# Performance work log

Hardware: AMD Instinct MI355X
Metric: run time of the kernel (lower is better)

## Reference

```python
import jax, jax.numpy as jnp
import numpy as np

LN_EPS = 1e-5

def _layernorm(x, g, b):
    m = jnp.mean(x, axis=-1, keepdims=True)
    v = jnp.var(x, axis=-1, keepdims=True)
    return (x - m) * jax.lax.rsqrt(v + LN_EPS) * g + b

def setup_inputs() -> dict:
    key = jax.random.key(0)
    ks = jax.random.split(key, 12)
    BT, D, OH, OW = 32, 768, 28, 43
    N, NFB, NFC = 12, 1024, 256
    s = 0.02
    return {
        "roi_feature": jax.random.normal(ks[0], (BT * N, NFB), jnp.float32),
        "image_feature": jax.random.normal(ks[1], (BT, D, OH, OW), jnp.float32),
        "conv_w": jax.random.normal(ks[2], (NFC, D), jnp.float32) * s,
        "conv_b": jnp.zeros((NFC,), jnp.float32),
        "emb_w": jax.random.normal(ks[3], (NFC, NFB), jnp.float32) * s,
        "emb_b": jnp.zeros((NFC,), jnp.float32),
        "ln1_g": jnp.ones((NFC,), jnp.float32),
        "ln1_b": jnp.zeros((NFC,), jnp.float32),
        "ffn_w1": jax.random.normal(ks[4], (NFC, NFC), jnp.float32) * s,
        "ffn_b1": jnp.zeros((NFC,), jnp.float32),
        "ffn_w2": jax.random.normal(ks[5], (NFC, NFC), jnp.float32) * s,
        "ffn_b2": jnp.zeros((NFC,), jnp.float32),
        "ln2_g": jnp.ones((NFC,), jnp.float32),
        "ln2_b": jnp.zeros((NFC,), jnp.float32),
        "N": 12,
        "layer_id": 1,
    }

def reference(roi_feature, image_feature, conv_w, conv_b, emb_w, emb_b,
              ln1_g, ln1_b, ffn_w1, ffn_b1, ffn_w2, ffn_b2, ln2_g, ln2_b,
              N, layer_id):
    BT, D, OH, OW = image_feature.shape
    NFC = conv_w.shape[0]
    # 1x1 conv == channel GEMM: [BT, D, OH, OW] -> [BT, NFC, OH*OW]
    img = jnp.einsum('bchw,oc->bohw', image_feature, conv_w) + conv_b[None, :, None, None]
    img = img.reshape(BT, NFC, OH * OW)                       # [BT, NFC, P]
    # roi embedding: [BT*N, NFB] -> [BT, N, NFC]
    emb = (roi_feature @ emb_w.T + emb_b).reshape(BT, N, NFC)
    # cross-attention: logits [BT, N, P], softmax over spatial positions
    logits = jnp.einsum('bnc,bcp->bnp', emb, img)
    A = jax.nn.softmax(logits, axis=2)
    ctx = jnp.einsum('bnp,bcp->bnc', A, img).reshape(BT * N, NFC)
    # residual + LN1 (dropout is identity at inference)
    x = _layernorm(ctx + emb.reshape(BT * N, NFC), ln1_g, ln1_b)
    # FFN residual + LN2
    h = jax.nn.relu(x @ ffn_w1.T + ffn_b1) @ ffn_w2.T + ffn_b2
    return _layernorm(x + h, ln2_g, ln2_b)
```

## Files before the change

### kernel.cpp

```cpp
#include <hip/hip_runtime.h>
#include <hip/hip_bf16.h>
#include <stdint.h>

typedef __hip_bfloat16 bf16;
typedef __attribute__((ext_vector_type(8))) __bf16 frag8;
typedef __attribute__((ext_vector_type(4))) float f32x4;

__device__ inline float wred_sum(float v) {
#pragma unroll
  for (int o = 32; o; o >>= 1) v += __shfl_down(v, o);
  return v;
}
__device__ inline float wred_max(float v) {
#pragma unroll
  for (int o = 32; o; o >>= 1) v = fmaxf(v, __shfl_down(v, o));
  return v;
}
__device__ inline unsigned short bits_of(bf16 h) { return *(unsigned short*)&h; }
__device__ inline frag8 cvt8(float4 lo, float4 hi) {
  union { frag8 f; unsigned short u[8]; } r;
  r.u[0] = bits_of(__float2bfloat16(lo.x));
  r.u[1] = bits_of(__float2bfloat16(lo.y));
  r.u[2] = bits_of(__float2bfloat16(lo.z));
  r.u[3] = bits_of(__float2bfloat16(lo.w));
  r.u[4] = bits_of(__float2bfloat16(hi.x));
  r.u[5] = bits_of(__float2bfloat16(hi.y));
  r.u[6] = bits_of(__float2bfloat16(hi.z));
  r.u[7] = bits_of(__float2bfloat16(hi.w));
  return r.f;
}

__global__ __launch_bounds__(256) void wt_k(const float* __restrict__ W,
                                            bf16* __restrict__ Wt) {
  __shared__ float t[32][33];
  int c0 = blockIdx.x * 32, o0 = blockIdx.y * 32;
  int tx = threadIdx.x & 31, ty = threadIdx.x >> 5;
#pragma unroll
  for (int i = 0; i < 4; ++i)
    t[ty + i * 8][tx] = W[(long)(o0 + ty + i * 8) * 768 + c0 + tx];
  __syncthreads();
#pragma unroll
  for (int i = 0; i < 4; ++i)
    Wt[(long)(c0 + ty + i * 8) * 256 + o0 + tx] = __float2bfloat16(t[tx][ty + i * 8]);
}

template <int NT, bool AF32, bool BF32, bool RELU, bool OUT_BF16, bool BIAS>
__global__ __launch_bounds__(64) void gemm_sm2(const void* __restrict__ Av,
                                               const void* __restrict__ Bv,
                                               void* __restrict__ C, int K, int ldc,
                                               const float* __restrict__ bias) {
  int n0 = blockIdx.x * (16 * NT), m0 = blockIdx.y * 64;
  int lr = threadIdx.x & 15, kg = threadIdx.x >> 4;
  f32x4 acc[4][NT] = {};
#pragma unroll 2
  for (int k0 = 0; k0 < K; k0 += 32) {
    frag8 af[4], bv[NT];
#pragma unroll
    for (int mi = 0; mi < 4; ++mi) {
      long row = m0 + mi * 16 + lr;
      if constexpr (AF32) {
        const float* ap = (const float*)Av + row * K + k0 + kg * 8;
        af[mi] = cvt8(*(const float4*)ap, *(const float4*)(ap + 4));
      } else {
        af[mi] = *(const frag8*)((const bf16*)Av + row * K + k0 + kg * 8);
      }
    }
#pragma unroll
    for (int ni = 0; ni < NT; ++ni) {
      long row = n0 + ni * 16 + lr;
      if constexpr (BF32) {
        const float* bp = (const float*)Bv + row * K + k0 + kg * 8;
        bv[ni] = cvt8(*(const float4*)bp, *(const float4*)(bp + 4));
      } else {
        bv[ni] = *(const frag8*)((const bf16*)Bv + row * K + k0 + kg * 8);
      }
    }
#pragma unroll
    for (int mi = 0; mi < 4; ++mi)
#pragma unroll
      for (int ni = 0; ni < NT; ++ni)
        acc[mi][ni] = __builtin_amdgcn_mfma_f32_16x16x32_bf16(af[mi], bv[ni],
                                                              acc[mi][ni], 0, 0, 0);
  }
#pragma unroll
  for (int mi = 0; mi < 4; ++mi)
#pragma unroll
    for (int ni = 0; ni < NT; ++ni)
#pragma unroll
      for (int j = 0; j < 4; ++j) {
        int row = m0 + mi * 16 + kg * 4 + j;
        int col = n0 + ni * 16 + lr;
        float v = acc[mi][ni][j];
        if (BIAS) v += bias[col];
        if (RELU) v = fmaxf(v, 0.f);
        long idx = (long)row * ldc + col;
        if constexpr (OUT_BF16) ((bf16*)C)[idx] = __float2bfloat16(v);
        else ((float*)C)[idx] = v;
      }
}

__global__ __launch_bounds__(256) void logits2(const float* __restrict__ X,
                                               const float* __restrict__ embW,
                                               float* __restrict__ lgt) {
  int px = blockIdx.x, cs = blockIdx.y, b = blockIdx.z;
  __shared__ float e[12 * 96];
  for (int i = threadIdx.x; i < 12 * 96; i += 256)
    e[i] = embW[((long)b * 12 + i / 96) * 768 + cs * 96 + (i % 96)];
  __syncthreads();
  int slot = px * 256 + threadIdx.x;
  if (slot >= 301) return;
  int p = slot * 4;
  const float* xb = X + ((long)b * 768 + cs * 96) * 1204 + p;
  float a0[12], a1[12], a2[12], a3[12];
#pragma unroll
  for (int n = 0; n < 12; ++n) { a0[n] = a1[n] = a2[n] = a3[n] = 0.f; }
#pragma unroll 4
  for (int c = 0; c < 96; ++c) {
    float4 xq = *(const float4*)(xb + (long)c * 1204);
#pragma unroll
    for (int n = 0; n < 12; ++n) {
      float en = e[n * 96 + c];
      a0[n] += en * xq.x; a1[n] += en * xq.y;
      a2[n] += en * xq.z; a3[n] += en * xq.w;
    }
  }
#pragma unroll
  for (int n = 0; n < 12; ++n)
    *(float4*)&lgt[((long)cs * 384 + b * 12 + n) * 1204 + p] =
        make_float4(a0[n], a1[n], a2[n], a3[n]);
}

__global__ __launch_bounds__(256) void softmax2(const float* __restrict__ lgt,
                                                bf16* __restrict__ am) {
  const long PS = (long)384 * 1204;
  int b = blockIdx.x, n = blockIdx.y, tid = threadIdx.x;
  bf16* row = am + ((long)b * 16 + n) * 1280;
  if (n >= 12) {
    for (int i = tid; i < 1280; i += 256) row[i] = __float2bfloat16(0.f);
    return;
  }
  const float* l0 = lgt + ((long)b * 12 + n) * 1204;
  float vals[5];
  float m = -3.0e38f;
#pragma unroll
  for (int i = 0; i < 5; ++i) {
    int pp = tid + i * 256;
    if (pp < 1204) {
      float v = 0.f;
#pragma unroll
      for (int q = 0; q < 8; ++q) v += l0[q * PS + pp];
      vals[i] = v;
    } else {
      vals[i] = -3.0e38f;
    }
    m = fmaxf(m, vals[i]);
  }
  m = wred_max(m);
  __shared__ float rd[4];
  int w = tid >> 6, lane = tid & 63;
  if (lane == 0) rd[w] = m;
  __syncthreads();
  m = fmaxf(fmaxf(rd[0], rd[1]), fmaxf(rd[2], rd[3]));
  float s = 0.f;
#pragma unroll
  for (int i = 0; i < 5; ++i) {
    int pp = tid + i * 256;
    vals[i] = (pp < 1204) ? __expf(vals[i] - m) : 0.f;
    s += vals[i];
  }
  s = wred_sum(s);
  __syncthreads();
  if (lane == 0) rd[w] = s;
  __syncthreads();
  s = rd[0] + rd[1] + rd[2] + rd[3];
  float inv = 1.f / s;
#pragma unroll
  for (int i = 0; i < 5; ++i) {
    int pp = tid + i * 256;
    row[pp] = __float2bfloat16((pp < 1204) ? vals[i] * inv : 0.f);
  }
}

__global__ __launch_bounds__(64) void ctx_a(const float* __restrict__ X,
                                            const bf16* __restrict__ am,
                                            float* __restrict__ Yp) {
  int ct = blockIdx.x, kc = blockIdx.y, b = blockIdx.z;
  int c0 = ct * 64;
  int kst = kc * 256, kend = min(kst + 256, 1204);
  int lr = threadIdx.x & 15, kg = threadIdx.x >> 4;
  f32x4 acc[4] = {};
  for (int k0 = kst; k0 < kend; k0 += 32) {
    frag8 bv = *(const frag8*)(am + ((long)b * 16 + lr) * 1280 + k0 + kg * 8);
    bool full = (k0 + 32 <= 1204);
#pragma unroll
    for (int mi = 0; mi < 4; ++mi) {
      const float* ap = X + ((long)b * 768 + c0 + mi * 16 + lr) * 1204 + k0 + kg * 8;
      frag8 av;
      if (full) {
        av = cvt8(*(const float4*)ap, *(const float4*)(ap + 4));
      } else {
        float t[8];
#pragma unroll
        for (int j = 0; j < 8; ++j)
          t[j] = (k0 + kg * 8 + j < 1204) ? ap[j] : 0.f;
        av = cvt8(make_float4(t[0], t[1], t[2], t[3]),
                  make_float4(t[4], t[5], t[6], t[7]));
      }
      acc[mi] = __builtin_amdgcn_mfma_f32_16x16x32_bf16(av, bv, acc[mi], 0, 0, 0);
    }
  }
  if (lr < 12) {
#pragma unroll
    for (int mi = 0; mi < 4; ++mi) {
      long base = (((long)kc * 32 + b) * 12 + lr) * 768 + c0 + mi * 16 + kg * 4;
      *(float4*)&Yp[base] = make_float4(acc[mi][0], acc[mi][1], acc[mi][2], acc[mi][3]);
    }
  }
}

__global__ __launch_bounds__(256) void red_y(const float* __restrict__ Yp,
                                             bf16* __restrict__ Ysum) {
  const long QS = (long)32 * 12 * 768;
  long i = ((long)blockIdx.x * 256 + threadIdx.x) * 4;
  if (i >= QS) return;
  float4 v = *(const float4*)(Yp + i);
#pragma unroll
  for (int q = 1; q < 5; ++q) {
    float4 u = *(const float4*)(Yp + q * QS + i);
    v.x += u.x; v.y += u.y; v.z += u.z; v.w += u.w;
  }
  union { ushort4 s; bf16 h[4]; } o;
  o.h[0] = __float2bfloat16(v.x);
  o.h[1] = __float2bfloat16(v.y);
  o.h[2] = __float2bfloat16(v.z);
  o.h[3] = __float2bfloat16(v.w);
  *(ushort4*)(Ysum + i) = o.s;
}

__global__ __launch_bounds__(256) void ln_k(const float* __restrict__ a,
                                            const float* __restrict__ bb,
                                            const float* __restrict__ g,
                                            const float* __restrict__ be,
                                            float* __restrict__ of) {
  int r = blockIdx.x, c = threadIdx.x;
  long idx = (long)r * 256 + c;
  float v = a[idx] + bb[idx];
  float s = wred_sum(v);
  float s2 = wred_sum(v * v);
  __shared__ float r1[4], r2[4];
  int w = c >> 6, lane = c & 63;
  if (lane == 0) { r1[w] = s; r2[w] = s2; }
  __syncthreads();
  float st = r1[0] + r1[1] + r1[2] + r1[3];
  float s2t = r2[0] + r2[1] + r2[2] + r2[3];
  float mean = st * (1.f / 256.f);
  float var = s2t * (1.f / 256.f) - mean * mean;
  float rs = rsqrtf(var + 1e-5f);
  of[idx] = (v - mean) * rs * g[c] + be[c];
}

extern "C" void kernel_launch(void* const* d_in, const int* in_sizes, int n_in,
                              void* d_out, int out_size, void* d_ws, size_t ws_size,
                              hipStream_t stream) {
  const float* roi   = (const float*)d_in[0];
  const float* imgf  = (const float*)d_in[1];
  const float* convw = (const float*)d_in[2];
  const float* convb = (const float*)d_in[3];
  const float* embw  = (const float*)d_in[4];
  const float* embb  = (const float*)d_in[5];
  const float* ln1g  = (const float*)d_in[6];
  const float* ln1b  = (const float*)d_in[7];
  const float* w1    = (const float*)d_in[8];
  const float* b1    = (const float*)d_in[9];
  const float* w2    = (const float*)d_in[10];
  const float* b2    = (const float*)d_in[11];
  const float* ln2g  = (const float*)d_in[12];
  const float* ln2b  = (const float*)d_in[13];
  float* out = (float*)d_out;

  char* p = (char*)d_ws;
  size_t off = 0;
  auto take = [&](size_t sz) -> char* {
    char* r = p + off;
    off += (sz + 255) & ~(size_t)255;
    return r;
  };
  float* emb  = (float*)take((size_t)384 * 256 * 4);
  bf16*  Wt   = (bf16*)take((size_t)768 * 256 * 2);
  float* embW = (float*)take((size_t)384 * 768 * 4);
  float* lgt  = (float*)take((size_t)8 * 384 * 1204 * 4);
  bf16*  am   = (bf16*)take((size_t)32 * 16 * 1280 * 2);
  float* Yp   = (float*)take((size_t)5 * 32 * 12 * 768 * 4);
  bf16*  Ysum = (bf16*)take((size_t)384 * 768 * 2);
  float* ctxf = (float*)take((size_t)384 * 256 * 4);
  float* x    = (float*)take((size_t)384 * 256 * 4);
  bf16*  h1   = (bf16*)take((size_t)384 * 256 * 2);
  float* h    = (float*)take((size_t)384 * 256 * 4);

  gemm_sm2<1, true, true, false, false, true><<<dim3(16, 6), 64, 0, stream>>>(
      roi, embw, emb, 1024, 256, embb);
  wt_k<<<dim3(24, 8), 256, 0, stream>>>(convw, Wt);
  gemm_sm2<1, true, false, false, false, false><<<dim3(48, 6), 64, 0, stream>>>(
      emb, Wt, embW, 256, 768, nullptr);
  logits2<<<dim3(2, 8, 32), 256, 0, stream>>>(imgf, embW, lgt);
  softmax2<<<dim3(32, 16), 256, 0, stream>>>(lgt, am);
  ctx_a<<<dim3(12, 5, 32), 64, 0, stream>>>(imgf, am, Yp);
  red_y<<<288, 256, 0, stream>>>(Yp, Ysum);
  gemm_sm2<1, false, true, false, false, true><<<dim3(16, 6), 64, 0, stream>>>(
      Ysum, convw, ctxf, 768, 256, convb);
  ln_k<<<384, 256, 0, stream>>>(ctxf, emb, ln1g, ln1b, x);
  gemm_sm2<1, true, true, true, true, true><<<dim3(16, 6), 64, 0, stream>>>(
      x, w1, h1, 256, 256, b1);
  gemm_sm2<1, false, true, false, false, true><<<dim3(16, 6), 64, 0, stream>>>(
      h1, w2, h, 256, 256, b2);
  ln_k<<<384, 256, 0, stream>>>(h, x, ln2g, ln2b, out);
}
```

Measured before the change: 137.8 us.

## Fuse tail GEMMs and layernorms into one kernel; split logits channels finer

Replaces the five tail launches (conv GEMM, LN1, two FFN GEMMs, LN2) with one tail_k kernel. Each block handles 16 rows, keeps intermediates in LDS and converts the fp32 weights to bf16 on the fly. The logits kernel now splits channels into 16 chunks of 48 with 320-thread blocks (one block per batch and chunk instead of two), so softmax sums 16 partials. This removes launch overhead and global round-trips for the tail, but tail_k runs only 24 blocks, which may underuse the GPU, and the logits change doubles the partial-sum traffic.

```diff
diff --git a/kernel.cpp b/kernel.cpp
--- a/kernel.cpp
+++ b/kernel.cpp
@@ -44,17 +44,17 @@
     Wt[(long)(c0 + ty + i * 8) * 256 + o0 + tx] = __float2bfloat16(t[tx][ty + i * 8]);
 }
 
-template <int NT, bool AF32, bool BF32, bool RELU, bool OUT_BF16, bool BIAS>
+template <bool AF32, bool BF32, bool BIAS>
 __global__ __launch_bounds__(64) void gemm_sm2(const void* __restrict__ Av,
                                                const void* __restrict__ Bv,
-                                               void* __restrict__ C, int K, int ldc,
+                                               float* __restrict__ C, int K, int ldc,
                                                const float* __restrict__ bias) {
-  int n0 = blockIdx.x * (16 * NT), m0 = blockIdx.y * 64;
+  int n0 = blockIdx.x * 16, m0 = blockIdx.y * 64;
   int lr = threadIdx.x & 15, kg = threadIdx.x >> 4;
-  f32x4 acc[4][NT] = {};
+  f32x4 acc[4] = {};
 #pragma unroll 2
   for (int k0 = 0; k0 < K; k0 += 32) {
-    frag8 af[4], bv[NT];
+    frag8 af[4], bv;
 #pragma unroll
     for (int mi = 0; mi < 4; ++mi) {
       long row = m0 + mi * 16 + lr;
@@ -65,61 +65,52 @@
         af[mi] = *(const frag8*)((const bf16*)Av + row * K + k0 + kg * 8);
       }
     }
-#pragma unroll
-    for (int ni = 0; ni < NT; ++ni) {
-      long row = n0 + ni * 16 + lr;
+    {
+      long row = n0 + lr;
       if constexpr (BF32) {
         const float* bp = (const float*)Bv + row * K + k0 + kg * 8;
-        bv[ni] = cvt8(*(const float4*)bp, *(const float4*)(bp + 4));
+        bv = cvt8(*(const float4*)bp, *(const float4*)(bp + 4));
       } else {
-        bv[ni] = *(const frag8*)((const bf16*)Bv + row * K + k0 + kg * 8);
+        bv = *(const frag8*)((const bf16*)Bv + row * K + k0 + kg * 8);
       }
     }
 #pragma unroll
     for (int mi = 0; mi < 4; ++mi)
-#pragma unroll
-      for (int ni = 0; ni < NT; ++ni)
-        acc[mi][ni] = __builtin_amdgcn_mfma_f32_16x16x32_bf16(af[mi], bv[ni],
-                                                              acc[mi][ni], 0, 0, 0);
+      acc[mi] = __builtin_amdgcn_mfma_f32_16x16x32_bf16(af[mi], bv, acc[mi], 0, 0, 0);
   }
 #pragma unroll
   for (int mi = 0; mi < 4; ++mi)
 #pragma unroll
-    for (int ni = 0; ni < NT; ++ni)
-#pragma unroll
-      for (int j = 0; j < 4; ++j) {
-        int row = m0 + mi * 16 + kg * 4 + j;
-        int col = n0 + ni * 16 + lr;
-        float v = acc[mi][ni][j];
-        if (BIAS) v += bias[col];
-        if (RELU) v = fmaxf(v, 0.f);
-        long idx = (long)row * ldc + col;
-        if constexpr (OUT_BF16) ((bf16*)C)[idx] = __float2bfloat16(v);
-        else ((float*)C)[idx] = v;
-      }
-}
-
-__global__ __launch_bounds__(256) void logits2(const float* __restrict__ X,
+    for (int j = 0; j < 4; ++j) {
+      int row = m0 + mi * 16 + kg * 4 + j;
+      int col = n0 + lr;
+      float v = acc[mi][j];
+      if (BIAS) v += bias[col];
+      C[(long)row * ldc + col] = v;
+    }
+}
+
+__global__ __launch_bounds__(320) void logits2(const float* __restrict__ X,
                                                const float* __restrict__ embW,
                                                float* __restrict__ lgt) {
-  int px = blockIdx.x, cs = blockIdx.y, b = blockIdx.z;
-  __shared__ float e[12 * 96];
-  for (int i = threadIdx.x; i < 12 * 96; i += 256)
-    e[i] = embW[((long)b * 12 + i / 96) * 768 + cs * 96 + (i % 96)];
-  __syncthreads();
-  int slot = px * 256 + threadIdx.x;
+  int cs = blockIdx.x, b = blockIdx.y;
+  __shared__ float e[12 * 48];
+  for (int i = threadIdx.x; i < 12 * 48; i += 320)
+    e[i] = embW[((long)b * 12 + i / 48) * 768 + cs * 48 + (i % 48)];
+  __syncthreads();
+  int slot = threadIdx.x;
   if (slot >= 301) return;
   int p = slot * 4;
-  const float* xb = X + ((long)b * 768 + cs * 96) * 1204 + p;
+  const float* xb = X + ((long)b * 768 + cs * 48) * 1204 + p;
   float a0[12], a1[12], a2[12], a3[12];
 #pragma unroll
   for (int n = 0; n < 12; ++n) { a0[n] = a1[n] = a2[n] = a3[n] = 0.f; }
 #pragma unroll 4
-  for (int c = 0; c < 96; ++c) {
+  for (int c = 0; c < 48; ++c) {
     float4 xq = *(const float4*)(xb + (long)c * 1204);
 #pragma unroll
     for (int n = 0; n < 12; ++n) {
-      float en = e[n * 96 + c];
+      float en = e[n * 48 + c];
       a0[n] += en * xq.x; a1[n] += en * xq.y;
       a2[n] += en * xq.z; a3[n] += en * xq.w;
     }
@@ -148,7 +139,7 @@
     if (pp < 1204) {
       float v = 0.f;
 #pragma unroll
-      for (int q = 0; q < 8; ++q) v += l0[q * PS + pp];
+      for (int q = 0; q < 16; ++q) v += l0[q * PS + pp];
       vals[i] = v;
     } else {
       vals[i] = -3.0e38f;
@@ -237,26 +228,135 @@
   *(ushort4*)(Ysum + i) = o.s;
 }
 
-__global__ __launch_bounds__(256) void ln_k(const float* __restrict__ a,
-                                            const float* __restrict__ bb,
-                                            const float* __restrict__ g,
-                                            const float* __restrict__ be,
-                                            float* __restrict__ of) {
-  int r = blockIdx.x, c = threadIdx.x;
-  long idx = (long)r * 256 + c;
-  float v = a[idx] + bb[idx];
-  float s = wred_sum(v);
-  float s2 = wred_sum(v * v);
-  __shared__ float r1[4], r2[4];
-  int w = c >> 6, lane = c & 63;
-  if (lane == 0) { r1[w] = s; r2[w] = s2; }
-  __syncthreads();
-  float st = r1[0] + r1[1] + r1[2] + r1[3];
-  float s2t = r2[0] + r2[1] + r2[2] + r2[3];
-  float mean = st * (1.f / 256.f);
-  float var = s2t * (1.f / 256.f) - mean * mean;
-  float rs = rsqrtf(var + 1e-5f);
-  of[idx] = (v - mean) * rs * g[c] + be[c];
+__global__ __launch_bounds__(256) void tail_k(
+    const bf16* __restrict__ Ysum, const float* __restrict__ convw,
+    const float* __restrict__ convb, const float* __restrict__ emb,
+    const float* __restrict__ ln1g, const float* __restrict__ ln1b,
+    const float* __restrict__ w1, const float* __restrict__ b1,
+    const float* __restrict__ w2, const float* __restrict__ b2,
+    const float* __restrict__ ln2g, const float* __restrict__ ln2b,
+    float* __restrict__ out) {
+  int r0 = blockIdx.x * 16;
+  __shared__ __align__(16) bf16 A_l[16][776];
+  __shared__ float x_l[16][260];
+  __shared__ __align__(16) bf16 xb_l[16][264];
+  __shared__ __align__(16) bf16 h1_l[16][264];
+  int tid = threadIdx.x;
+  int lane = tid & 63, w = tid >> 6;
+  int lr = lane & 15, kg = lane >> 4;
+  int n0 = w * 64;
+  for (int i = tid; i < 1536; i += 256) {
+    int r = i / 96, c8 = (i % 96) * 8;
+    *(uint4*)&A_l[r][c8] = *(const uint4*)(Ysum + (long)(r0 + r) * 768 + c8);
+  }
+  __syncthreads();
+  {
+    f32x4 acc[4] = {};
+    for (int k0 = 0; k0 < 768; k0 += 32) {
+      frag8 af = *(const frag8*)&A_l[lr][k0 + kg * 8];
+#pragma unroll
+      for (int ni = 0; ni < 4; ++ni) {
+        const float* bp = convw + (long)(n0 + ni * 16 + lr) * 768 + k0 + kg * 8;
+        frag8 bv = cvt8(*(const float4*)bp, *(const float4*)(bp + 4));
+        acc[ni] = __builtin_amdgcn_mfma_f32_16x16x32_bf16(af, bv, acc[ni], 0, 0, 0);
+      }
+    }
+#pragma unroll
+    for (int ni = 0; ni < 4; ++ni)
+#pragma unroll
+      for (int j = 0; j < 4; ++j) {
+        int row = kg * 4 + j, col = n0 + ni * 16 + lr;
+        x_l[row][col] = acc[ni][j] + convb[col] + emb[(long)(r0 + row) * 256 + col];
+      }
+  }
+  __syncthreads();
+  {
+    int r = tid >> 4, seg = tid & 15;
+    float s = 0.f, s2 = 0.f;
+#pragma unroll
+    for (int i = 0; i < 16; ++i) {
+      float v = x_l[r][seg * 16 + i];
+      s += v; s2 += v * v;
+    }
+#pragma unroll
+    for (int msk = 1; msk < 16; msk <<= 1) {
+      s += __shfl_xor(s, msk);
+      s2 += __shfl_xor(s2, msk);
+    }
+    float mean = s * (1.f / 256.f);
+    float var = s2 * (1.f / 256.f) - mean * mean;
+    float rs = rsqrtf(var + 1e-5f);
+#pragma unroll
+    for (int i = 0; i < 16; ++i) {
+      int c = seg * 16 + i;
+      float y = (x_l[r][c] - mean) * rs * ln1g[c] + ln1b[c];
+      x_l[r][c] = y;
+      xb_l[r][c] = __float2bfloat16(y);
+    }
+  }
+  __syncthreads();
+  {
+    f32x4 acc[4] = {};
+    for (int k0 = 0; k0 < 256; k0 += 32) {
+      frag8 af = *(const frag8*)&xb_l[lr][k0 + kg * 8];
+#pragma unroll
+      for (int ni = 0; ni < 4; ++ni) {
+        const float* bp = w1 + (long)(n0 + ni * 16 + lr) * 256 + k0 + kg * 8;
+        frag8 bv = cvt8(*(const float4*)bp, *(const float4*)(bp + 4));
+        acc[ni] = __builtin_amdgcn_mfma_f32_16x16x32_bf16(af, bv, acc[ni], 0, 0, 0);
+      }
+    }
+#pragma unroll
+    for (int ni = 0; ni < 4; ++ni)
+#pragma unroll
+      for (int j = 0; j < 4; ++j) {
+        int row = kg * 4 + j, col = n0 + ni * 16 + lr;
+        h1_l[row][col] = __float2bfloat16(fmaxf(acc[ni][j] + b1[col], 0.f));
+      }
+  }
+  __syncthreads();
+  {
+    f32x4 acc[4] = {};
+    for (int k0 = 0; k0 < 256; k0 += 32) {
+      frag8 af = *(const frag8*)&h1_l[lr][k0 + kg * 8];
+#pragma unroll
+      for (int ni = 0; ni < 4; ++ni) {
+        const float* bp = w2 + (long)(n0 + ni * 16 + lr) * 256 + k0 + kg * 8;
+        frag8 bv = cvt8(*(const float4*)bp, *(const float4*)(bp + 4));
+        acc[ni] = __builtin_amdgcn_mfma_f32_16x16x32_bf16(af, bv, acc[ni], 0, 0, 0);
+      }
+    }
+#pragma unroll
+    for (int ni = 0; ni < 4; ++ni)
+#pragma unroll
+      for (int j = 0; j < 4; ++j) {
+        int row = kg * 4 + j, col = n0 + ni * 16 + lr;
+        x_l[row][col] += acc[ni][j] + b2[col];
+      }
+  }
+  __syncthreads();
+  {
+    int r = tid >> 4, seg = tid & 15;
+    float s = 0.f, s2 = 0.f;
+#pragma unroll
+    for (int i = 0; i < 16; ++i) {
+      float v = x_l[r][seg * 16 + i];
+      s += v; s2 += v * v;
+    }
+#pragma unroll
+    for (int msk = 1; msk < 16; msk <<= 1) {
+      s += __shfl_xor(s, msk);
+      s2 += __shfl_xor(s2, msk);
+    }
+    float mean = s * (1.f / 256.f);
+    float var = s2 * (1.f / 256.f) - mean * mean;
+    float rs = rsqrtf(var + 1e-5f);
+#pragma unroll
+    for (int i = 0; i < 16; ++i) {
+      int c = seg * 16 + i;
+      out[(long)(r0 + r) * 256 + c] = (x_l[r][c] - mean) * rs * ln2g[c] + ln2b[c];
+    }
+  }
 }
 
 extern "C" void kernel_launch(void* const* d_in, const int* in_sizes, int n_in,
@@ -288,30 +388,20 @@
   float* emb  = (float*)take((size_t)384 * 256 * 4);
   bf16*  Wt   = (bf16*)take((size_t)768 * 256 * 2);
   float* embW = (float*)take((size_t)384 * 768 * 4);
-  float* lgt  = (float*)take((size_t)8 * 384 * 1204 * 4);
+  float* lgt  = (float*)take((size_t)16 * 384 * 1204 * 4);
   bf16*  am   = (bf16*)take((size_t)32 * 16 * 1280 * 2);
   float* Yp   = (float*)take((size_t)5 * 32 * 12 * 768 * 4);
   bf16*  Ysum = (bf16*)take((size_t)384 * 768 * 2);
-  float* ctxf = (float*)take((size_t)384 * 256 * 4);
-  float* x    = (float*)take((size_t)384 * 256 * 4);
-  bf16*  h1   = (bf16*)take((size_t)384 * 256 * 2);
-  float* h    = (float*)take((size_t)384 * 256 * 4);
-
-  gemm_sm2<1, true, true, false, false, true><<<dim3(16, 6), 64, 0, stream>>>(
+
+  gemm_sm2<true, true, true><<<dim3(16, 6), 64, 0, stream>>>(
       roi, embw, emb, 1024, 256, embb);
   wt_k<<<dim3(24, 8), 256, 0, stream>>>(convw, Wt);
-  gemm_sm2<1, true, false, false, false, false><<<dim3(48, 6), 64, 0, stream>>>(
+  gemm_sm2<true, false, false><<<dim3(48, 6), 64, 0, stream>>>(
       emb, Wt, embW, 256, 768, nullptr);
-  logits2<<<dim3(2, 8, 32), 256, 0, stream>>>(imgf, embW, lgt);
+  logits2<<<dim3(16, 32), 320, 0, stream>>>(imgf, embW, lgt);
   softmax2<<<dim3(32, 16), 256, 0, stream>>>(lgt, am);
   ctx_a<<<dim3(12, 5, 32), 64, 0, stream>>>(imgf, am, Yp);
   red_y<<<288, 256, 0, stream>>>(Yp, Ysum);
-  gemm_sm2<1, false, true, false, false, true><<<dim3(16, 6), 64, 0, stream>>>(
-      Ysum, convw, ctxf, 768, 256, convb);
-  ln_k<<<384, 256, 0, stream>>>(ctxf, emb, ln1g, ln1b, x);
-  gemm_sm2<1, true, true, true, true, true><<<dim3(16, 6), 64, 0, stream>>>(
-      x, w1, h1, 256, 256, b1);
-  gemm_sm2<1, false, true, false, false, true><<<dim3(16, 6), 64, 0, stream>>>(
-      h1, w2, h, 256, 256, b2);
-  ln_k<<<384, 256, 0, stream>>>(h, x, ln2g, ln2b, out);
-}
+  tail_k<<<24, 256, 0, stream>>>(Ysum, convw, convb, emb, ln1g, ln1b,
+                                 w1, b1, w2, b2, ln2g, ln2b, out);
+}
```

New measurement: 147.1 us. +6.7%, slower.
